# Kernel tuning notes

Hardware: AMD Instinct MI355X
Metric: run time of the kernel (lower is better)

The kernel has to match this reference:

```python
import jax, jax.numpy as jnp
import numpy as np

D_MODEL = 1024
B, N = 2, 4096
EPS = 1e-4


def setup_inputs() -> dict:
    key = jax.random.key(0)
    ks = jax.random.split(key, 8)
    s = 1.0 / np.sqrt(D_MODEL)
    return {
        "x": jax.random.normal(ks[0], (B, N, D_MODEL), dtype=jnp.float32),
        "Wq": jax.random.normal(ks[1], (D_MODEL, D_MODEL), dtype=jnp.float32) * s,
        "bq": jax.random.normal(ks[2], (D_MODEL,), dtype=jnp.float32) * 0.01,
        "Wk": jax.random.normal(ks[3], (D_MODEL, D_MODEL), dtype=jnp.float32) * s,
        "bk": jax.random.normal(ks[4], (D_MODEL,), dtype=jnp.float32) * 0.01,
        "Wv": jax.random.normal(ks[5], (D_MODEL, D_MODEL), dtype=jnp.float32) * s,
        "bv": jax.random.normal(ks[6], (D_MODEL,), dtype=jnp.float32) * 0.01,
        "alpha": jnp.float32(1.5),
        "lam": jnp.float32(12.0),
    }


def reference(x, Wq, bq, Wk, bk, Wv, bv, alpha, lam):
    # CSOCKernelAttention.forward
    Bb, n, d = x.shape
    # torch nn.Linear: y = x @ W.T + b
    q = jnp.einsum("bnd,ed->bne", x, Wq) + bq
    k = jnp.einsum("bnd,ed->bne", x, Wk) + bk
    v = jnp.einsum("bnd,ed->bne", x, Wv) + bv
    idx = jnp.arange(n, dtype=jnp.float32)
    r = jnp.abs(idx[:, None] - idx[None, :])  # [N, N]
    # K(r) = (r + eps)^(-|alpha|) * exp(-r / |lambda|)
    K = (r + EPS) ** (-jnp.abs(alpha)) * jnp.exp(-r / jnp.abs(lam))  # [N, N]
    logits = jnp.einsum("bqd,bkd->bqk", q, k) / jnp.sqrt(jnp.float32(d))
    logits = logits * K[None]
    attn = jax.nn.softmax(logits, axis=-1)
    out = jnp.einsum("bqk,bkd->bqd", attn, v)
    return (out, attn, K)
```

## Files before the change

### kernel.cpp

```cpp
#include <hip/hip_runtime.h>
#include <hip/hip_bf16.h>
#include <cstdint>
#include <cstddef>

#define D_MODEL 1024
#define SEQ_N   4096
#define BATCH   2
#define BAND    256
#define NELEM   ((size_t)BATCH * SEQ_N * D_MODEL)

typedef __attribute__((ext_vector_type(4))) float  floatx4;
typedef __attribute__((ext_vector_type(8))) short  short8;
typedef __attribute__((ext_vector_type(4))) short  short4v;

__device__ __forceinline__ unsigned short f2bf(float f) {
  unsigned u = __float_as_uint(f);
  u += 0x7FFFu + ((u >> 16) & 1u);
  return (unsigned short)(u >> 16);
}
__device__ __forceinline__ float bf2f(unsigned short u) {
  return __uint_as_float(((unsigned)u) << 16);
}

__global__ __launch_bounds__(256)
void fused_prep(const float* __restrict__ x,
                const float* __restrict__ Wq, const float* __restrict__ Wk,
                const float* __restrict__ Wv,
                const float* __restrict__ bq, const float* __restrict__ bk,
                const float* __restrict__ bv,
                const float* __restrict__ alpha_p, const float* __restrict__ lam_p,
                unsigned short* __restrict__ xb, unsigned short* __restrict__ wcat,
                float* __restrict__ bcat, float* __restrict__ K1d)
{
  int bid = blockIdx.x, tid = threadIdx.x;
  if (bid < 4096) {
    int i = bid * 256 + tid;
    const floatx4* s4 = (const floatx4*)x;
    floatx4 a = s4[i * 2], b = s4[i * 2 + 1];
    short8 pk;
    pk[0] = (short)f2bf(a[0]); pk[1] = (short)f2bf(a[1]);
    pk[2] = (short)f2bf(a[2]); pk[3] = (short)f2bf(a[3]);
    pk[4] = (short)f2bf(b[0]); pk[5] = (short)f2bf(b[1]);
    pk[6] = (short)f2bf(b[2]); pk[7] = (short)f2bf(b[3]);
    *(short8*)(xb + (size_t)i * 8) = pk;
  } else if (bid < 5632) {
    int u = bid - 4096;
    int z = u >> 9;
    int i = (u & 511) * 256 + tid;
    const float* src = (z == 0) ? Wq : (z == 1) ? Wk : Wv;
    unsigned short* d = wcat + (size_t)z * (D_MODEL * D_MODEL);
    const floatx4* s4 = (const floatx4*)src;
    floatx4 a = s4[i * 2], b = s4[i * 2 + 1];
    short8 pk;
    pk[0] = (short)f2bf(a[0]); pk[1] = (short)f2bf(a[1]);
    pk[2] = (short)f2bf(a[2]); pk[3] = (short)f2bf(a[3]);
    pk[4] = (short)f2bf(b[0]); pk[5] = (short)f2bf(b[1]);
    pk[6] = (short)f2bf(b[2]); pk[7] = (short)f2bf(b[3]);
    *(short8*)(d + (size_t)i * 8) = pk;
  } else {
    int t = (bid - 5632) * 256 + tid;
    if (t < SEQ_N) {
      float a   = fabsf(alpha_p[0]);
      float lam = fabsf(lam_p[0]);
      float rf  = (float)t;
      K1d[t] = powf(rf + 1e-4f, -a) * expf(-rf / lam);
    }
    int v = t - SEQ_N;
    if (v >= 0 && v < 3 * D_MODEL) {
      bcat[v] = (v < D_MODEL) ? bq[v]
              : (v < 2 * D_MODEL) ? bk[v - D_MODEL]
              : bv[v - 2 * D_MODEL];
    }
  }
}

__global__ void k1d_kernel(float* __restrict__ K1d,
                           const float* __restrict__ alpha_p,
                           const float* __restrict__ lam_p) {
  int r = blockIdx.x * blockDim.x + threadIdx.x;
  if (r >= SEQ_N) return;
  float a   = fabsf(alpha_p[0]);
  float lam = fabsf(lam_p[0]);
  float rf  = (float)r;
  K1d[r] = powf(rf + 1e-4f, -a) * expf(-rf / lam);
}

__global__ __launch_bounds__(256) void writeK_kernel(float* __restrict__ Kout,
                                                     const float* __restrict__ K1d) {
  size_t t = (size_t)blockIdx.x * 256 + threadIdx.x;
  size_t f = t * 4;
  int i = (int)(f >> 12);
  int j = (int)(f & 4095);
  floatx4 v;
#pragma unroll
  for (int e = 0; e < 4; ++e) {
    int d = i - (j + e); d = d < 0 ? -d : d;
    v[e] = K1d[d];
  }
  __builtin_nontemporal_store(v, (floatx4*)(Kout + f));
}

__global__ __launch_bounds__(256)
void qkv_qk(const unsigned short* __restrict__ xb,
            const unsigned short* __restrict__ wcat,
            const float* __restrict__ bcat,
            unsigned short* __restrict__ qb)
{
  __shared__ unsigned short As[128 * 32];
  __shared__ unsigned short Bs[128 * 32];
  const int tid = threadIdx.x, lane = tid & 63, wave = tid >> 6;

  int gx = (int)gridDim.x, gy = (int)gridDim.y;
  int total = gx * gy;
  int flat  = (int)blockIdx.y * gx + (int)blockIdx.x;
  int w     = (flat & 7) * (total >> 3) + (flat >> 3);
  int bx = w % gx, by = w / gx;
  const int bm0 = by * 128;
  const int bn0 = bx * 128;
  const int wm = (wave >> 1) * 64, wn = (wave & 1) * 64;

  floatx4 acc[4][4] = {};
  for (int k0 = 0; k0 < D_MODEL; k0 += 32) {
#pragma unroll
    for (int t = 0; t < 2; ++t) {
      int bu = wave * 64 + t * 256;
      int u  = bu + lane;
      const unsigned short* srcA = xb + (size_t)(bm0 + (u >> 2)) * D_MODEL + k0 + (u & 3) * 8;
      __builtin_amdgcn_global_load_lds((const __attribute__((address_space(1))) void*)srcA,
                                       (__attribute__((address_space(3))) void*)(As + bu * 8), 16, 0, 0);
      const unsigned short* srcB = wcat + (size_t)(bn0 + (u >> 2)) * D_MODEL + k0 + (u & 3) * 8;
      __builtin_amdgcn_global_load_lds((const __attribute__((address_space(1))) void*)srcB,
                                       (__attribute__((address_space(3))) void*)(Bs + bu * 8), 16, 0, 0);
    }
    __syncthreads();
    short8 af[4], bf[4];
#pragma unroll
    for (int i = 0; i < 4; ++i)
      af[i] = *(const short8*)(As + (wm + i * 16 + (lane & 15)) * 32 + (lane >> 4) * 8);
#pragma unroll
    for (int j = 0; j < 4; ++j)
      bf[j] = *(const short8*)(Bs + (wn + j * 16 + (lane & 15)) * 32 + (lane >> 4) * 8);
#pragma unroll
    for (int i = 0; i < 4; ++i)
#pragma unroll
      for (int j = 0; j < 4; ++j)
        acc[i][j] = __builtin_amdgcn_mfma_f32_16x16x32_bf16(bf[j], af[i], acc[i][j], 0, 0, 0);
    __syncthreads();
  }

#pragma unroll
  for (int i = 0; i < 4; ++i) {
#pragma unroll
    for (int j = 0; j < 4; ++j) {
      int xrow = bm0 + wm + i * 16 + (lane & 15);
      int n0   = bn0 + wn + j * 16 + (lane >> 4) * 4;
      floatx4 b4 = *(const floatx4*)(bcat + n0);
      unsigned short* C = qb + ((n0 >= D_MODEL) ? NELEM : 0);
      short4v pk;
#pragma unroll
      for (int r = 0; r < 4; ++r) pk[r] = (short)f2bf(acc[i][j][r] + b4[r]);
      *(short4v*)(C + (size_t)xrow * D_MODEL + (n0 & (D_MODEL - 1))) = pk;
    }
  }
}

__global__ __launch_bounds__(256)
void qkv_v(const unsigned short* __restrict__ xb,
           const unsigned short* __restrict__ wcat,
           const float* __restrict__ bcat,
           unsigned short* __restrict__ vT)
{
  __shared__ unsigned short As[128 * 32];
  __shared__ unsigned short Bs[128 * 32];
  const int tid = threadIdx.x, lane = tid & 63, wave = tid >> 6;

  int gx = (int)gridDim.x, gy = (int)gridDim.y;
  int total = gx * gy;
  int flat  = (int)blockIdx.y * gx + (int)blockIdx.x;
  int w     = (flat & 7) * (total >> 3) + (flat >> 3);
  int bx = w % gx, by = w / gx;
  const int bm0 = by * 128;
  const int bn0 = bx * 128;
  const int wm = (wave >> 1) * 64, wn = (wave & 1) * 64;
  const unsigned short* Wg = wcat + (size_t)2048 * D_MODEL;

  floatx4 acc[4][4] = {};
  for (int k0 = 0; k0 < D_MODEL; k0 += 32) {
#pragma unroll
    for (int t = 0; t < 2; ++t) {
      int bu = wave * 64 + t * 256;
      int u  = bu + lane;
      const unsigned short* srcA = xb + (size_t)(bm0 + (u >> 2)) * D_MODEL + k0 + (u & 3) * 8;
      __builtin_amdgcn_global_load_lds((const __attribute__((address_space(1))) void*)srcA,
                                       (__attribute__((address_space(3))) void*)(As + bu * 8), 16, 0, 0);
      const unsigned short* srcB = Wg + (size_t)(bn0 + (u >> 2)) * D_MODEL + k0 + (u & 3) * 8;
      __builtin_amdgcn_global_load_lds((const __attribute__((address_space(1))) void*)srcB,
                                       (__attribute__((address_space(3))) void*)(Bs + bu * 8), 16, 0, 0);
    }
    __syncthreads();
    short8 af[4], bf[4];
#pragma unroll
    for (int i = 0; i < 4; ++i)
      af[i] = *(const short8*)(As + (wm + i * 16 + (lane & 15)) * 32 + (lane >> 4) * 8);
#pragma unroll
    for (int j = 0; j < 4; ++j)
      bf[j] = *(const short8*)(Bs + (wn + j * 16 + (lane & 15)) * 32 + (lane >> 4) * 8);
#pragma unroll
    for (int i = 0; i < 4; ++i)
#pragma unroll
      for (int j = 0; j < 4; ++j)
        acc[i][j] = __builtin_amdgcn_mfma_f32_16x16x32_bf16(af[i], bf[j], acc[i][j], 0, 0, 0);
    __syncthreads();
  }

#pragma unroll
  for (int i = 0; i < 4; ++i) {
#pragma unroll
    for (int j = 0; j < 4; ++j) {
      int e     = bn0 + wn + j * 16 + (lane & 15);
      int rbase = bm0 + wm + i * 16 + (lane >> 4) * 4;
      float b = bcat[2048 + e];
      short4v pk;
#pragma unroll
      for (int r = 0; r < 4; ++r) pk[r] = (short)f2bf(acc[i][j][r] + b);
      *(short4v*)(vT + (size_t)e * (BATCH * SEQ_N) + rbase) = pk;
    }
  }
}

__global__ __launch_bounds__(256)
void band_logits(const unsigned short* __restrict__ Q,
                 const unsigned short* __restrict__ Kb,
                 float* __restrict__ Sband,
                 const float* __restrict__ K1d)
{
  __shared__ unsigned short As[64 * 32];
  __shared__ unsigned short Bs[128 * 32];
  const int tid = threadIdx.x, lane = tid & 63, wave = tid >> 6;
  const int bx = blockIdx.x;
  const int g  = blockIdx.y;
  const int z  = blockIdx.z;
  const int bm0 = g * 64;
  const int bn0 = g * 64 - 64 + bx * 128;
  const int wm = (wave >> 1) * 32, wn = (wave & 1) * 64;

  const unsigned short* Ag = Q  + (size_t)z * SEQ_N * D_MODEL;
  const unsigned short* Bg = Kb + (size_t)z * SEQ_N * D_MODEL;

  floatx4 acc[2][4] = {};
  for (int k0 = 0; k0 < D_MODEL; k0 += 32) {
    {
      int bu = wave * 64;
      int u  = bu + lane;
      const unsigned short* srcA = Ag + (size_t)(bm0 + (u >> 2)) * D_MODEL + k0 + (u & 3) * 8;
      __builtin_amdgcn_global_load_lds((const __attribute__((address_space(1))) void*)srcA,
                                       (__attribute__((address_space(3))) void*)(As + bu * 8), 16, 0, 0);
    }
#pragma unroll
    for (int t = 0; t < 2; ++t) {
      int bu = wave * 64 + t * 256;
      int u  = bu + lane;
      const unsigned short* srcB = Bg + (long)(bn0 + (u >> 2)) * D_MODEL + k0 + (u & 3) * 8;
      __builtin_amdgcn_global_load_lds((const __attribute__((address_space(1))) void*)srcB,
                                       (__attribute__((address_space(3))) void*)(Bs + bu * 8), 16, 0, 0);
    }
    __syncthreads();
    short8 af[2], bf[4];
#pragma unroll
    for (int i = 0; i < 2; ++i)
      af[i] = *(const short8*)(As + (wm + i * 16 + (lane & 15)) * 32 + (lane >> 4) * 8);
#pragma unroll
    for (int j = 0; j < 4; ++j)
      bf[j] = *(const short8*)(Bs + (wn + j * 16 + (lane & 15)) * 32 + (lane >> 4) * 8);
#pragma unroll
    for (int i = 0; i < 2; ++i)
#pragma unroll
      for (int j = 0; j < 4; ++j)
        acc[i][j] = __builtin_amdgcn_mfma_f32_16x16x32_bf16(af[i], bf[j], acc[i][j], 0, 0, 0);
    __syncthreads();
  }

  float* Cb = Sband + ((size_t)z * SEQ_N + bm0) * BAND + bx * 128;
#pragma unroll
  for (int i = 0; i < 2; ++i) {
#pragma unroll
    for (int j = 0; j < 4; ++j) {
      int cl  = wn + j * 16 + (lane & 15);
      int rl0 = wm + i * 16 + (lane >> 4) * 4;
#pragma unroll
      for (int r = 0; r < 4; ++r) {
        int col = bn0 + cl;
        int d = (bm0 + rl0 + r) - col; d = d < 0 ? -d : d;
        float v = ((unsigned)col < (unsigned)SEQ_N) ? acc[i][j][r] * 0.03125f * K1d[d] : 0.f;
        Cb[(size_t)(rl0 + r) * BAND + cl] = v;
      }
    }
  }
}

__global__ __launch_bounds__(256)
void softmax_band(const float* __restrict__ Sband,
                  float* __restrict__ attn,
                  unsigned short* __restrict__ Pb,
                  float* __restrict__ c_arr)
{
  __shared__ float lds_e[4][BAND];
  const int lane = threadIdx.x & 63, wave = threadIdx.x >> 6;
  const int gi = blockIdx.x * 4 + wave;
  const int ii = gi & (SEQ_N - 1);
  const int g  = ii >> 6;
  const int cbase = g * 64 - 64;
  const float* S = Sband + (size_t)gi * BAND;

  float sv[4];
  float m = 0.0f;
#pragma unroll
  for (int j = 0; j < 4; ++j) {
    int t = j * 64 + lane;
    int col = cbase + t;
    sv[j] = S[t];
    if ((unsigned)col < (unsigned)SEQ_N) m = fmaxf(m, sv[j]);
  }
#pragma unroll
  for (int o = 32; o; o >>= 1) m = fmaxf(m, __shfl_xor(m, o));

  float s = 0.f;
#pragma unroll
  for (int j = 0; j < 4; ++j) {
    int t = j * 64 + lane;
    int col = cbase + t;
    float e = ((unsigned)col < (unsigned)SEQ_N) ? __expf(sv[j] - m) : 0.f;
    sv[j] = e;
    s += e;
  }
#pragma unroll
  for (int o = 32; o; o >>= 1) s += __shfl_xor(s, o);

  int n_valid = BAND - ((g == 0) ? 64 : 0) - ((g == 63) ? 64 : 0);
  float efar  = __expf(-m);
  float denom = s + (float)(SEQ_N - n_valid) * efar;
  float inv   = 1.0f / denom;
  float c     = efar * inv;

  unsigned short* prow = Pb + (size_t)gi * BAND;
#pragma unroll
  for (int j = 0; j < 4; ++j) {
    int t = j * 64 + lane;
    float p = sv[j] * inv;
    lds_e[wave][t] = p;
    int col = cbase + t;
    prow[t] = ((unsigned)col < (unsigned)SEQ_N) ? f2bf(p - c) : (unsigned short)0;
  }
  if (lane == 0) c_arr[gi] = c;

  float* arow = attn + (size_t)gi * SEQ_N;
#pragma unroll
  for (int jj = 0; jj < 16; ++jj) {
    int col0 = jj * 256 + lane * 4;
    floatx4 o;
#pragma unroll
    for (int e = 0; e < 4; ++e) {
      int t = col0 + e - cbase;
      o[e] = ((unsigned)t < (unsigned)BAND) ? lds_e[wave][t] : c;
    }
    __builtin_nontemporal_store(o, (floatx4*)(arow + col0));
  }
}

__global__ __launch_bounds__(256)
void colsumv_kernel(const unsigned short* __restrict__ vT, float* __restrict__ colsumV) {
  const int lane = threadIdx.x & 63, wave = threadIdx.x >> 6;
  const int idx = blockIdx.x * 4 + wave;
  const int d = idx >> 1, b = idx & 1;
  const unsigned short* p = vT + (size_t)d * (BATCH * SEQ_N) + b * SEQ_N;
  float s = 0.f;
#pragma unroll
  for (int it = 0; it < 8; ++it) {
    short8 v = *(const short8*)(p + (size_t)(it * 512 + lane * 8));
#pragma unroll
    for (int e = 0; e < 8; ++e) s += bf2f((unsigned short)v[e]);
  }
#pragma unroll
  for (int o = 32; o; o >>= 1) s += __shfl_xor(s, o);
  if (lane == 0) colsumV[b * D_MODEL + d] = s;
}

__global__ __launch_bounds__(256)
void band_pv(const unsigned short* __restrict__ Pb,
             const unsigned short* __restrict__ vT,
             const float* __restrict__ c_arr,
             const float* __restrict__ colsumV,
             float* __restrict__ outp)
{
  __shared__ unsigned short As[64 * 32];
  __shared__ unsigned short Bs[128 * 32];
  const int tid = threadIdx.x, lane = tid & 63, wave = tid >> 6;
  const int bx = blockIdx.x;
  const int g  = blockIdx.y;
  const int z  = blockIdx.z;
  const int bm0 = g * 64;
  const int bn0 = bx * 128;
  const int wm = (wave >> 1) * 32, wn = (wave & 1) * 64;

  const unsigned short* Ag = Pb + ((size_t)z * SEQ_N + bm0) * BAND;
  const unsigned short* Bg = vT + (long)z * SEQ_N + (long)bm0 - 64;

  floatx4 acc[2][4] = {};
  for (int k0 = 0; k0 < BAND; k0 += 32) {
    {
      int bu = wave * 64;
      int u  = bu + lane;
      const unsigned short* srcA = Ag + (size_t)(u >> 2) * BAND + k0 + (u & 3) * 8;
      __builtin_amdgcn_global_load_lds((const __attribute__((address_space(1))) void*)srcA,
                                       (__attribute__((address_space(3))) void*)(As + bu * 8), 16, 0, 0);
    }
#pragma unroll
    for (int t = 0; t < 2; ++t) {
      int bu = wave * 64 + t * 256;
      int u  = bu + lane;
      const unsigned short* srcB = Bg + (size_t)(bn0 + (u >> 2)) * (BATCH * SEQ_N) + k0 + (u & 3) * 8;
      __builtin_amdgcn_global_load_lds((const __attribute__((address_space(1))) void*)srcB,
                                       (__attribute__((address_space(3))) void*)(Bs + bu * 8), 16, 0, 0);
    }
    __syncthreads();
    short8 af[2], bf[4];
#pragma unroll
    for (int i = 0; i < 2; ++i)
      af[i] = *(const short8*)(As + (wm + i * 16 + (lane & 15)) * 32 + (lane >> 4) * 8);
#pragma unroll
    for (int j = 0; j < 4; ++j)
      bf[j] = *(const short8*)(Bs + (wn + j * 16 + (lane & 15)) * 32 + (lane >> 4) * 8);
#pragma unroll
    for (int i = 0; i < 2; ++i)
#pragma unroll
      for (int j = 0; j < 4; ++j)
        acc[i][j] = __builtin_amdgcn_mfma_f32_16x16x32_bf16(af[i], bf[j], acc[i][j], 0, 0, 0);
    __syncthreads();
  }

#pragma unroll
  for (int i = 0; i < 2; ++i) {
#pragma unroll
    for (int j = 0; j < 4; ++j) {
      int col   = bn0 + wn + j * 16 + (lane & 15);
      int rbase = bm0 + wm + i * 16 + (lane >> 4) * 4;
      float csv = colsumV[z * D_MODEL + col];
#pragma unroll
      for (int r = 0; r < 4; ++r) {
        int row = rbase + r;
        float o = acc[i][j][r] + c_arr[(size_t)z * SEQ_N + row] * csv;
        __builtin_nontemporal_store(o, outp + ((size_t)z * SEQ_N + row) * D_MODEL + col);
      }
    }
  }
}

#define BM 128
#define BN 128
#define BK 32

template<int ASRC, int BSRC, int EPI>
__global__ __launch_bounds__(256)
void gemm_bt(const void* __restrict__ Ap_, int lda, long sA,
             const void* __restrict__ Bp_, int ldb, long sB,
             void* __restrict__ Cp_, int ldc, long sC,
             int K, const float* __restrict__ bias,
             const float* __restrict__ K1d)
{
  __shared__ unsigned short As[BM * BK];
  __shared__ unsigned short Bs[BN * BK];
  const int tid  = threadIdx.x;
  const int lane = tid & 63;
  const int wave = tid >> 6;

  int gx = (int)gridDim.x, gy = (int)gridDim.y;
  int total = gx * gy * (int)gridDim.z;
  int flat  = (int)blockIdx.z * gx * gy + (int)blockIdx.y * gx + (int)blockIdx.x;
  int w     = (flat & 7) * (total >> 3) + (flat >> 3);
  int bx = w % gx;
  int t_ = w / gx;
  int by = t_ % gy;
  int z  = t_ / gy;

  const int bm0  = by * BM;
  const int bn0  = bx * BN;
  const int wm   = (wave >> 1) * 64;
  const int wn   = (wave & 1) * 64;

  floatx4 acc[4][4] = {};

  const unsigned short* Agb = (const unsigned short*)Ap_ + (size_t)z * (size_t)sA;
  const float*          Agf = (const float*)Ap_          + (size_t)z * (size_t)sA;
  const unsigned short* Bgb = (const unsigned short*)Bp_ + (size_t)z * (size_t)sB;
  const float*          Bgf = (const float*)Bp_          + (size_t)z * (size_t)sB;

  for (int k0 = 0; k0 < K; k0 += BK) {
    if constexpr (ASRC == 0) {
#pragma unroll
      for (int t = 0; t < 2; ++t) {
        int bu = wave * 64 + t * 256;
        int u  = bu + lane;
        const unsigned short* src = Agb + (size_t)(bm0 + (u >> 2)) * lda + k0 + (u & 3) * 8;
        __builtin_amdgcn_global_load_lds((const __attribute__((address_space(1))) void*)src,
                                         (__attribute__((address_space(3))) void*)(As + bu * 8),
                                         16, 0, 0);
      }
    } else {
#pragma unroll
      for (int t = 0; t < 2; ++t) {
        int u = tid + t * 256;
        const float* src = Agf + (size_t)(bm0 + (u >> 2)) * lda + k0 + (u & 3) * 8;
        floatx4 x0 = *(const floatx4*)src;
        floatx4 x1 = *(const floatx4*)(src + 4);
        short8 pk;
        pk[0] = (short)f2bf(x0[0]); pk[1] = (short)f2bf(x0[1]);
        pk[2] = (short)f2bf(x0[2]); pk[3] = (short)f2bf(x0[3]);
        pk[4] = (short)f2bf(x1[0]); pk[5] = (short)f2bf(x1[1]);
        pk[6] = (short)f2bf(x1[2]); pk[7] = (short)f2bf(x1[3]);
        *(short8*)(As + u * 8) = pk;
      }
    }
    if constexpr (BSRC == 0) {
#pragma unroll
      for (int t = 0; t < 2; ++t) {
        int bu = wave * 64 + t * 256;
        int u  = bu + lane;
        const unsigned short* src = Bgb + (size_t)(bn0 + (u >> 2)) * ldb + k0 + (u & 3) * 8;
        __builtin_amdgcn_global_load_lds((const __attribute__((address_space(1))) void*)src,
                                         (__attribute__((address_space(3))) void*)(Bs + bu * 8),
                                         16, 0, 0);
      }
    } else {
#pragma unroll
      for (int t = 0; t < 2; ++t) {
        int u = tid + t * 256;
        const float* src = Bgf + (size_t)(bn0 + (u >> 2)) * ldb + k0 + (u & 3) * 8;
        floatx4 x0 = *(const floatx4*)src;
        floatx4 x1 = *(const floatx4*)(src + 4);
        short8 pk;
        pk[0] = (short)f2bf(x0[0]); pk[1] = (short)f2bf(x0[1]);
        pk[2] = (short)f2bf(x0[2]); pk[3] = (short)f2bf(x0[3]);
        pk[4] = (short)f2bf(x1[0]); pk[5] = (short)f2bf(x1[1]);
        pk[6] = (short)f2bf(x1[2]); pk[7] = (short)f2bf(x1[3]);
        *(short8*)(Bs + u * 8) = pk;
      }
    }
    __syncthreads();

    short8 af[4], bf[4];
#pragma unroll
    for (int i = 0; i < 4; ++i)
      af[i] = *(const short8*)(As + (wm + i * 16 + (lane & 15)) * BK + (lane >> 4) * 8);
#pragma unroll
    for (int j = 0; j < 4; ++j)
      bf[j] = *(const short8*)(Bs + (wn + j * 16 + (lane & 15)) * BK + (lane >> 4) * 8);
#pragma unroll
    for (int i = 0; i < 4; ++i)
#pragma unroll
      for (int j = 0; j < 4; ++j)
        acc[i][j] = __builtin_amdgcn_mfma_f32_16x16x32_bf16(af[i], bf[j], acc[i][j], 0, 0, 0);
    __syncthreads();
  }

  const int col0 = bn0 + wn;
  const int row0 = bm0 + wm;
#pragma unroll
  for (int i = 0; i < 4; ++i) {
#pragma unroll
    for (int j = 0; j < 4; ++j) {
      int col   = col0 + j * 16 + (lane & 15);
      int rbase = row0 + i * 16 + (lane >> 4) * 4;
      if constexpr (EPI == 0) {
        unsigned short* C = (unsigned short*)Cp_ + (size_t)z * (size_t)sC;
        float b = bias[col];
#pragma unroll
        for (int r = 0; r < 4; ++r)
          C[(size_t)(rbase + r) * ldc + col] = f2bf(acc[i][j][r] + b);
      } else if constexpr (EPI == 1) {
        unsigned short* C = (unsigned short*)Cp_ + (size_t)z * (size_t)sC;
#pragma unroll
        for (int r = 0; r < 4; ++r)
          C[(size_t)(rbase + r) * ldc + col] = f2bf(acc[i][j][r] + bias[rbase + r]);
      } else if constexpr (EPI == 2) {
        float* C = (float*)Cp_ + (size_t)z * (size_t)sC;
#pragma unroll
        for (int r = 0; r < 4; ++r) {
          int row = rbase + r;
          int d = row - col; d = d < 0 ? -d : d;
          C[(size_t)row * ldc + col] = acc[i][j][r] * 0.03125f * K1d[d];
        }
      } else {
        float* C = (float*)Cp_ + (size_t)z * (size_t)sC;
#pragma unroll
        for (int r = 0; r < 4; ++r)
          C[(size_t)(rbase + r) * ldc + col] = acc[i][j][r];
      }
    }
  }
}

__global__ __launch_bounds__(256)
void softmax_kernel(float* __restrict__ attn) {
  const int tid = threadIdx.x;
  float* p = attn + (size_t)blockIdx.x * SEQ_N;
  floatx4* p4 = (floatx4*)p;
  floatx4 x[4];
  float m = -3.402823466e+38f;
#pragma unroll
  for (int c = 0; c < 4; ++c) {
    x[c] = p4[tid + c * 256];
    m = fmaxf(m, fmaxf(fmaxf(x[c][0], x[c][1]), fmaxf(x[c][2], x[c][3])));
  }
#pragma unroll
  for (int o = 32; o; o >>= 1) m = fmaxf(m, __shfl_xor(m, o));
  __shared__ float redm[4], reds[4];
  if ((tid & 63) == 0) redm[tid >> 6] = m;
  __syncthreads();
  m = fmaxf(fmaxf(redm[0], redm[1]), fmaxf(redm[2], redm[3]));
  float s = 0.f;
#pragma unroll
  for (int c = 0; c < 4; ++c)
#pragma unroll
    for (int e = 0; e < 4; ++e) {
      float t = __expf(x[c][e] - m);
      x[c][e] = t;
      s += t;
    }
#pragma unroll
  for (int o = 32; o; o >>= 1) s += __shfl_xor(s, o);
  if ((tid & 63) == 0) reds[tid >> 6] = s;
  __syncthreads();
  s = reds[0] + reds[1] + reds[2] + reds[3];
  float inv = 1.0f / s;
#pragma unroll
  for (int c = 0; c < 4; ++c) {
    floatx4 y;
#pragma unroll
    for (int e = 0; e < 4; ++e) y[e] = x[c][e] * inv;
    p4[tid + c * 256] = y;
  }
}

extern "C" void kernel_launch(void* const* d_in, const int* in_sizes, int n_in,
                              void* d_out, int out_size, void* d_ws, size_t ws_size,
                              hipStream_t stream) {
  const float* x     = (const float*)d_in[0];
  const float* Wq    = (const float*)d_in[1];
  const float* bq    = (const float*)d_in[2];
  const float* Wk    = (const float*)d_in[3];
  const float* bk    = (const float*)d_in[4];
  const float* Wv    = (const float*)d_in[5];
  const float* bv    = (const float*)d_in[6];
  const float* alpha = (const float*)d_in[7];
  const float* lam   = (const float*)d_in[8];

  float* outp  = (float*)d_out;
  float* attnp = outp + (size_t)BATCH * SEQ_N * D_MODEL;
  float* Kp    = attnp + (size_t)BATCH * SEQ_N * SEQ_N;

  char* ws = (char*)d_ws;
  float* K1d = (float*)ws;
  unsigned short* qb  = (unsigned short*)(ws + 16384);
  unsigned short* kb  = qb + NELEM;
  unsigned short* vT  = kb + NELEM;
  unsigned short* xb  = vT + NELEM;
  unsigned short* wcat = xb + NELEM;
  float* Sband        = (float*)(wcat + (size_t)3 * D_MODEL * D_MODEL);
  unsigned short* Pb  = (unsigned short*)(Sband + (size_t)BATCH * SEQ_N * BAND);
  float* c_arr        = (float*)(Pb + (size_t)BATCH * SEQ_N * BAND);
  float* colsumV      = c_arr + (size_t)BATCH * SEQ_N;
  float* bcat         = colsumV + (size_t)BATCH * D_MODEL;

  size_t need = (size_t)((char*)(bcat + 3 * D_MODEL) - ws);
  const bool fast = ws_size >= need;

  if (fast) {
    fused_prep<<<5660, 256, 0, stream>>>(x, Wq, Wk, Wv, bq, bk, bv, alpha, lam,
                                         xb, wcat, bcat, K1d);
    writeK_kernel<<<(SEQ_N * SEQ_N / 4) / 256, 256, 0, stream>>>(Kp, K1d);

    qkv_qk<<<dim3(16, 64), 256, 0, stream>>>(xb, wcat, bcat, qb);
    qkv_v <<<dim3(8, 64), 256, 0, stream>>>(xb, wcat, bcat, vT);

    colsumv_kernel<<<BATCH * D_MODEL / 4, 256, 0, stream>>>(vT, colsumV);
    band_logits<<<dim3(2, SEQ_N / 64, BATCH), 256, 0, stream>>>(qb, kb, Sband, K1d);
    softmax_band<<<BATCH * SEQ_N / 4, 256, 0, stream>>>(Sband, attnp, Pb, c_arr);
    band_pv<<<dim3(D_MODEL / 128, SEQ_N / 64, BATCH), 256, 0, stream>>>(
        Pb, vT, c_arr, colsumV, outp);
  } else {
    k1d_kernel<<<16, 256, 0, stream>>>(K1d, alpha, lam);
    writeK_kernel<<<(SEQ_N * SEQ_N / 4) / 256, 256, 0, stream>>>(Kp, K1d);
    gemm_bt<1, 1, 0><<<dim3(D_MODEL / BN, BATCH * SEQ_N / BM, 1), 256, 0, stream>>>(
        x, D_MODEL, 0, Wq, D_MODEL, 0, qb, D_MODEL, 0, D_MODEL, bq, nullptr);
    gemm_bt<1, 1, 0><<<dim3(D_MODEL / BN, BATCH * SEQ_N / BM, 1), 256, 0, stream>>>(
        x, D_MODEL, 0, Wk, D_MODEL, 0, kb, D_MODEL, 0, D_MODEL, bk, nullptr);
    gemm_bt<1, 1, 1><<<dim3(BATCH * SEQ_N / BN, D_MODEL / BM, 1), 256, 0, stream>>>(
        Wv, D_MODEL, 0, x, D_MODEL, 0, vT, BATCH * SEQ_N, 0, D_MODEL, bv, nullptr);
    gemm_bt<0, 0, 2><<<dim3(SEQ_N / BN, SEQ_N / BM, BATCH), 256, 0, stream>>>(
        qb, D_MODEL, (long)SEQ_N * D_MODEL, kb, D_MODEL, (long)SEQ_N * D_MODEL,
        attnp, SEQ_N, (long)SEQ_N * SEQ_N, D_MODEL, nullptr, K1d);
    softmax_kernel<<<BATCH * SEQ_N, 256, 0, stream>>>(attnp);
    gemm_bt<1, 0, 3><<<dim3(D_MODEL / BN, SEQ_N / BM, BATCH), 256, 0, stream>>>(
        attnp, SEQ_N, (long)SEQ_N * SEQ_N, vT, BATCH * SEQ_N, (long)SEQ_N,
        outp, D_MODEL, (long)SEQ_N * D_MODEL, SEQ_N, nullptr, nullptr);
  }
}
```

Baseline: 182.1 us.

## Fold Wq·Wk into combined matrix to drop separate K projection

Rewrites the logits as x·(Wq^T Wk)·x^T plus bias-derived terms: a small 1024x1024 GEMM forms M = Wk^T Wq, a vector-matrix kernel builds bq·Wk and bk·Wq, and a per-row rho term carries the remaining bias contributions. The QKV projection becomes one GEMM producing U = xM + bias and V, and band_logits now multiplies U against x directly, adding rho. This removes one full projection GEMM over the sequence and the K buffer, at the cost of extra small kernels and bf16 rounding of the fused matrix, which could change accuracy.

```diff
diff --git a/kernel.cpp b/kernel.cpp
--- a/kernel.cpp
+++ b/kernel.cpp
@@ -25,13 +25,16 @@
 __global__ __launch_bounds__(256)
 void fused_prep(const float* __restrict__ x,
                 const float* __restrict__ Wq, const float* __restrict__ Wk,
-                const float* __restrict__ Wv,
-                const float* __restrict__ bq, const float* __restrict__ bk,
-                const float* __restrict__ bv,
+                const float* __restrict__ Wv, const float* __restrict__ bv,
                 const float* __restrict__ alpha_p, const float* __restrict__ lam_p,
-                unsigned short* __restrict__ xb, unsigned short* __restrict__ wcat,
-                float* __restrict__ bcat, float* __restrict__ K1d)
-{
+                unsigned short* __restrict__ xb,
+                unsigned short* __restrict__ Bcat2,
+                unsigned short* __restrict__ wqT,
+                unsigned short* __restrict__ wkT,
+                float* __restrict__ bias2,
+                float* __restrict__ K1d)
+{
+  __shared__ unsigned short Tld[64][66];
   int bid = blockIdx.x, tid = threadIdx.x;
   if (bid < 4096) {
     int i = bid * 256 + tid;
@@ -43,22 +46,40 @@
     pk[4] = (short)f2bf(b[0]); pk[5] = (short)f2bf(b[1]);
     pk[6] = (short)f2bf(b[2]); pk[7] = (short)f2bf(b[3]);
     *(short8*)(xb + (size_t)i * 8) = pk;
-  } else if (bid < 5632) {
-    int u = bid - 4096;
-    int z = u >> 9;
-    int i = (u & 511) * 256 + tid;
-    const float* src = (z == 0) ? Wq : (z == 1) ? Wk : Wv;
-    unsigned short* d = wcat + (size_t)z * (D_MODEL * D_MODEL);
-    const floatx4* s4 = (const floatx4*)src;
+  } else if (bid < 4608) {
+    int i = (bid - 4096) * 256 + tid;
+    const floatx4* s4 = (const floatx4*)Wv;
     floatx4 a = s4[i * 2], b = s4[i * 2 + 1];
     short8 pk;
     pk[0] = (short)f2bf(a[0]); pk[1] = (short)f2bf(a[1]);
     pk[2] = (short)f2bf(a[2]); pk[3] = (short)f2bf(a[3]);
     pk[4] = (short)f2bf(b[0]); pk[5] = (short)f2bf(b[1]);
     pk[6] = (short)f2bf(b[2]); pk[7] = (short)f2bf(b[3]);
-    *(short8*)(d + (size_t)i * 8) = pk;
+    *(short8*)(Bcat2 + (size_t)D_MODEL * D_MODEL + (size_t)i * 8) = pk;
+  } else if (bid < 5120) {
+    int u = bid - 4608;
+    const float* src = (u < 256) ? Wq : Wk;
+    unsigned short* dst = (u < 256) ? wqT : wkT;
+    int t = u & 255;
+    int tr = t >> 4, tc = t & 15;
+    int rl = tid >> 2, cc = (tid & 3) * 16;
+    const float* sp = src + (size_t)(tr * 64 + rl) * D_MODEL + tc * 64 + cc;
+#pragma unroll
+    for (int q4 = 0; q4 < 4; ++q4) {
+      floatx4 v = *(const floatx4*)(sp + q4 * 4);
+#pragma unroll
+      for (int e = 0; e < 4; ++e) Tld[cc + q4 * 4 + e][rl] = f2bf(v[e]);
+    }
+    __syncthreads();
+    int cl = tid >> 2, rchunk = (tid & 3) * 16;
+    short8 o0, o1;
+#pragma unroll
+    for (int e = 0; e < 8; ++e) { o0[e] = (short)Tld[cl][rchunk + e]; o1[e] = (short)Tld[cl][rchunk + 8 + e]; }
+    unsigned short* dp = dst + (size_t)(tc * 64 + cl) * D_MODEL + tr * 64 + rchunk;
+    *(short8*)dp = o0;
+    *(short8*)(dp + 8) = o1;
   } else {
-    int t = (bid - 5632) * 256 + tid;
+    int t = (bid - 5120) * 256 + tid;
     if (t < SEQ_N) {
       float a   = fabsf(alpha_p[0]);
       float lam = fabsf(lam_p[0]);
@@ -66,12 +87,48 @@
       K1d[t] = powf(rf + 1e-4f, -a) * expf(-rf / lam);
     }
     int v = t - SEQ_N;
-    if (v >= 0 && v < 3 * D_MODEL) {
-      bcat[v] = (v < D_MODEL) ? bq[v]
-              : (v < 2 * D_MODEL) ? bk[v - D_MODEL]
-              : bv[v - 2 * D_MODEL];
-    }
-  }
+    if (v >= 0 && v < D_MODEL) bias2[D_MODEL + v] = bv[v];
+  }
+}
+
+__global__ __launch_bounds__(256)
+void vecmat_kernel(const float* __restrict__ bq, const float* __restrict__ Wk,
+                   const float* __restrict__ bk, const float* __restrict__ Wq,
+                   float* __restrict__ bias2, float* __restrict__ wqv)
+{
+  int z = blockIdx.z;
+  int d = blockIdx.x * 256 + threadIdx.x;
+  const float* b = z ? bk : bq;
+  const float* W = z ? Wq : Wk;
+  float s = 0.f;
+#pragma unroll 8
+  for (int e = 0; e < D_MODEL; ++e)
+    s += b[e] * W[(size_t)e * D_MODEL + d];
+  if (z) wqv[d] = s; else bias2[d] = s;
+}
+
+__global__ __launch_bounds__(256)
+void rho_kernel(const unsigned short* __restrict__ xb, const float* __restrict__ wqv,
+                const float* __restrict__ bq, const float* __restrict__ bk,
+                float* __restrict__ rho)
+{
+  const int lane = threadIdx.x & 63, wave = threadIdx.x >> 6;
+  const int gi = blockIdx.x * 4 + wave;
+  const unsigned short* xr = xb + (size_t)gi * D_MODEL + lane * 16;
+  float s1 = 0.f, s2 = 0.f;
+  short8 v0 = *(const short8*)xr, v1 = *(const short8*)(xr + 8);
+#pragma unroll
+  for (int e = 0; e < 8; ++e) {
+    s1 += bf2f((unsigned short)v0[e]) * wqv[lane * 16 + e];
+    s1 += bf2f((unsigned short)v1[e]) * wqv[lane * 16 + 8 + e];
+  }
+#pragma unroll
+  for (int e = 0; e < 16; ++e)
+    s2 += bq[lane * 16 + e] * bk[lane * 16 + e];
+  float s = s1 + s2;
+#pragma unroll
+  for (int o = 32; o; o >>= 1) s += __shfl_xor(s, o);
+  if (lane == 0) rho[gi] = s;
 }
 
 __global__ void k1d_kernel(float* __restrict__ K1d,
@@ -101,10 +158,67 @@
 }
 
 __global__ __launch_bounds__(256)
-void qkv_qk(const unsigned short* __restrict__ xb,
-            const unsigned short* __restrict__ wcat,
-            const float* __restrict__ bcat,
-            unsigned short* __restrict__ qb)
+void gemm64_mt(const unsigned short* __restrict__ A,
+               const unsigned short* __restrict__ B,
+               unsigned short* __restrict__ C)
+{
+  __shared__ unsigned short As[64 * 32];
+  __shared__ unsigned short Bs[64 * 32];
+  const int tid = threadIdx.x, lane = tid & 63, wave = tid >> 6;
+  int gx = (int)gridDim.x;
+  int total = gx * (int)gridDim.y;
+  int flat  = (int)blockIdx.y * gx + (int)blockIdx.x;
+  int w     = (flat & 7) * (total >> 3) + (flat >> 3);
+  int bx = w % gx, by = w / gx;
+  const int bm0 = by * 64, bn0 = bx * 64;
+  const int wm = (wave >> 1) * 32, wn = (wave & 1) * 32;
+
+  floatx4 acc[2][2] = {};
+  for (int k0 = 0; k0 < D_MODEL; k0 += 32) {
+    {
+      int bu = wave * 64;
+      int u  = bu + lane;
+      const unsigned short* srcA = A + (size_t)(bm0 + (u >> 2)) * D_MODEL + k0 + (u & 3) * 8;
+      __builtin_amdgcn_global_load_lds((const __attribute__((address_space(1))) void*)srcA,
+                                       (__attribute__((address_space(3))) void*)(As + bu * 8), 16, 0, 0);
+      const unsigned short* srcB = B + (size_t)(bn0 + (u >> 2)) * D_MODEL + k0 + (u & 3) * 8;
+      __builtin_amdgcn_global_load_lds((const __attribute__((address_space(1))) void*)srcB,
+                                       (__attribute__((address_space(3))) void*)(Bs + bu * 8), 16, 0, 0);
+    }
+    __syncthreads();
+    short8 af[2], bf[2];
+#pragma unroll
+    for (int i = 0; i < 2; ++i)
+      af[i] = *(const short8*)(As + (wm + i * 16 + (lane & 15)) * 32 + (lane >> 4) * 8);
+#pragma unroll
+    for (int j = 0; j < 2; ++j)
+      bf[j] = *(const short8*)(Bs + (wn + j * 16 + (lane & 15)) * 32 + (lane >> 4) * 8);
+#pragma unroll
+    for (int i = 0; i < 2; ++i)
+#pragma unroll
+      for (int j = 0; j < 2; ++j)
+        acc[i][j] = __builtin_amdgcn_mfma_f32_16x16x32_bf16(af[i], bf[j], acc[i][j], 0, 0, 0);
+    __syncthreads();
+  }
+#pragma unroll
+  for (int i = 0; i < 2; ++i) {
+#pragma unroll
+    for (int j = 0; j < 2; ++j) {
+      int col   = bn0 + wn + j * 16 + (lane & 15);
+      int rbase = bm0 + wm + i * 16 + (lane >> 4) * 4;
+#pragma unroll
+      for (int r = 0; r < 4; ++r)
+        C[(size_t)(rbase + r) * D_MODEL + col] = f2bf(acc[i][j][r]);
+    }
+  }
+}
+
+__global__ __launch_bounds__(256)
+void uv_gemm(const unsigned short* __restrict__ xb,
+             const unsigned short* __restrict__ Bcat2,
+             const float* __restrict__ bias2,
+             unsigned short* __restrict__ ub,
+             unsigned short* __restrict__ vT)
 {
   __shared__ unsigned short As[128 * 32];
   __shared__ unsigned short Bs[128 * 32];
@@ -118,6 +232,7 @@
   const int bm0 = by * 128;
   const int bn0 = bx * 128;
   const int wm = (wave >> 1) * 64, wn = (wave & 1) * 64;
+  const bool isU = (bn0 < D_MODEL);
 
   floatx4 acc[4][4] = {};
   for (int k0 = 0; k0 < D_MODEL; k0 += 32) {
@@ -128,7 +243,7 @@
       const unsigned short* srcA = xb + (size_t)(bm0 + (u >> 2)) * D_MODEL + k0 + (u & 3) * 8;
       __builtin_amdgcn_global_load_lds((const __attribute__((address_space(1))) void*)srcA,
                                        (__attribute__((address_space(3))) void*)(As + bu * 8), 16, 0, 0);
-      const unsigned short* srcB = wcat + (size_t)(bn0 + (u >> 2)) * D_MODEL + k0 + (u & 3) * 8;
+      const unsigned short* srcB = Bcat2 + (size_t)(bn0 + (u >> 2)) * D_MODEL + k0 + (u & 3) * 8;
       __builtin_amdgcn_global_load_lds((const __attribute__((address_space(1))) void*)srcB,
                                        (__attribute__((address_space(3))) void*)(Bs + bu * 8), 16, 0, 0);
     }
@@ -140,97 +255,58 @@
 #pragma unroll
     for (int j = 0; j < 4; ++j)
       bf[j] = *(const short8*)(Bs + (wn + j * 16 + (lane & 15)) * 32 + (lane >> 4) * 8);
-#pragma unroll
-    for (int i = 0; i < 4; ++i)
-#pragma unroll
-      for (int j = 0; j < 4; ++j)
-        acc[i][j] = __builtin_amdgcn_mfma_f32_16x16x32_bf16(bf[j], af[i], acc[i][j], 0, 0, 0);
-    __syncthreads();
-  }
-
-#pragma unroll
-  for (int i = 0; i < 4; ++i) {
-#pragma unroll
-    for (int j = 0; j < 4; ++j) {
-      int xrow = bm0 + wm + i * 16 + (lane & 15);
-      int n0   = bn0 + wn + j * 16 + (lane >> 4) * 4;
-      floatx4 b4 = *(const floatx4*)(bcat + n0);
-      unsigned short* C = qb + ((n0 >= D_MODEL) ? NELEM : 0);
-      short4v pk;
-#pragma unroll
-      for (int r = 0; r < 4; ++r) pk[r] = (short)f2bf(acc[i][j][r] + b4[r]);
-      *(short4v*)(C + (size_t)xrow * D_MODEL + (n0 & (D_MODEL - 1))) = pk;
-    }
-  }
-}
-
-__global__ __launch_bounds__(256)
-void qkv_v(const unsigned short* __restrict__ xb,
-           const unsigned short* __restrict__ wcat,
-           const float* __restrict__ bcat,
-           unsigned short* __restrict__ vT)
-{
-  __shared__ unsigned short As[128 * 32];
-  __shared__ unsigned short Bs[128 * 32];
-  const int tid = threadIdx.x, lane = tid & 63, wave = tid >> 6;
-
-  int gx = (int)gridDim.x, gy = (int)gridDim.y;
-  int total = gx * gy;
-  int flat  = (int)blockIdx.y * gx + (int)blockIdx.x;
-  int w     = (flat & 7) * (total >> 3) + (flat >> 3);
-  int bx = w % gx, by = w / gx;
-  const int bm0 = by * 128;
-  const int bn0 = bx * 128;
-  const int wm = (wave >> 1) * 64, wn = (wave & 1) * 64;
-  const unsigned short* Wg = wcat + (size_t)2048 * D_MODEL;
-
-  floatx4 acc[4][4] = {};
-  for (int k0 = 0; k0 < D_MODEL; k0 += 32) {
-#pragma unroll
-    for (int t = 0; t < 2; ++t) {
-      int bu = wave * 64 + t * 256;
-      int u  = bu + lane;
-      const unsigned short* srcA = xb + (size_t)(bm0 + (u >> 2)) * D_MODEL + k0 + (u & 3) * 8;
-      __builtin_amdgcn_global_load_lds((const __attribute__((address_space(1))) void*)srcA,
-                                       (__attribute__((address_space(3))) void*)(As + bu * 8), 16, 0, 0);
-      const unsigned short* srcB = Wg + (size_t)(bn0 + (u >> 2)) * D_MODEL + k0 + (u & 3) * 8;
-      __builtin_amdgcn_global_load_lds((const __attribute__((address_space(1))) void*)srcB,
-                                       (__attribute__((address_space(3))) void*)(Bs + bu * 8), 16, 0, 0);
-    }
-    __syncthreads();
-    short8 af[4], bf[4];
-#pragma unroll
-    for (int i = 0; i < 4; ++i)
-      af[i] = *(const short8*)(As + (wm + i * 16 + (lane & 15)) * 32 + (lane >> 4) * 8);
-#pragma unroll
-    for (int j = 0; j < 4; ++j)
-      bf[j] = *(const short8*)(Bs + (wn + j * 16 + (lane & 15)) * 32 + (lane >> 4) * 8);
-#pragma unroll
-    for (int i = 0; i < 4; ++i)
-#pragma unroll
-      for (int j = 0; j < 4; ++j)
-        acc[i][j] = __builtin_amdgcn_mfma_f32_16x16x32_bf16(af[i], bf[j], acc[i][j], 0, 0, 0);
-    __syncthreads();
-  }
-
-#pragma unroll
-  for (int i = 0; i < 4; ++i) {
-#pragma unroll
-    for (int j = 0; j < 4; ++j) {
-      int e     = bn0 + wn + j * 16 + (lane & 15);
-      int rbase = bm0 + wm + i * 16 + (lane >> 4) * 4;
-      float b = bcat[2048 + e];
-      short4v pk;
-#pragma unroll
-      for (int r = 0; r < 4; ++r) pk[r] = (short)f2bf(acc[i][j][r] + b);
-      *(short4v*)(vT + (size_t)e * (BATCH * SEQ_N) + rbase) = pk;
-    }
-  }
-}
-
-__global__ __launch_bounds__(256)
-void band_logits(const unsigned short* __restrict__ Q,
-                 const unsigned short* __restrict__ Kb,
+    if (isU) {
+#pragma unroll
+      for (int i = 0; i < 4; ++i)
+#pragma unroll
+        for (int j = 0; j < 4; ++j)
+          acc[i][j] = __builtin_amdgcn_mfma_f32_16x16x32_bf16(bf[j], af[i], acc[i][j], 0, 0, 0);
+    } else {
+#pragma unroll
+      for (int i = 0; i < 4; ++i)
+#pragma unroll
+        for (int j = 0; j < 4; ++j)
+          acc[i][j] = __builtin_amdgcn_mfma_f32_16x16x32_bf16(af[i], bf[j], acc[i][j], 0, 0, 0);
+    }
+    __syncthreads();
+  }
+
+  if (isU) {
+#pragma unroll
+    for (int i = 0; i < 4; ++i) {
+#pragma unroll
+      for (int j = 0; j < 4; ++j) {
+        int xrow = bm0 + wm + i * 16 + (lane & 15);
+        int n0   = bn0 + wn + j * 16 + (lane >> 4) * 4;
+        floatx4 b4 = *(const floatx4*)(bias2 + n0);
+        short4v pk;
+#pragma unroll
+        for (int r = 0; r < 4; ++r) pk[r] = (short)f2bf(acc[i][j][r] + b4[r]);
+        *(short4v*)(ub + (size_t)xrow * D_MODEL + n0) = pk;
+      }
+    }
+  } else {
+#pragma unroll
+    for (int i = 0; i < 4; ++i) {
+#pragma unroll
+      for (int j = 0; j < 4; ++j) {
+        int n     = bn0 + wn + j * 16 + (lane & 15);
+        int e     = n - D_MODEL;
+        int rbase = bm0 + wm + i * 16 + (lane >> 4) * 4;
+        float b = bias2[n];
+        short4v pk;
+#pragma unroll
+        for (int r = 0; r < 4; ++r) pk[r] = (short)f2bf(acc[i][j][r] + b);
+        *(short4v*)(vT + (size_t)e * (BATCH * SEQ_N) + rbase) = pk;
+      }
+    }
+  }
+}
+
+__global__ __launch_bounds__(256)
+void band_logits(const unsigned short* __restrict__ U,
+                 const unsigned short* __restrict__ Xb,
+                 const float* __restrict__ rho,
                  float* __restrict__ Sband,
                  const float* __restrict__ K1d)
 {
@@ -244,8 +320,8 @@
   const int bn0 = g * 64 - 64 + bx * 128;
   const int wm = (wave >> 1) * 32, wn = (wave & 1) * 64;
 
-  const unsigned short* Ag = Q  + (size_t)z * SEQ_N * D_MODEL;
-  const unsigned short* Bg = Kb + (size_t)z * SEQ_N * D_MODEL;
+  const unsigned short* Ag = U  + (size_t)z * SEQ_N * D_MODEL;
+  const unsigned short* Bg = Xb + (size_t)z * SEQ_N * D_MODEL;
 
   floatx4 acc[2][4] = {};
   for (int k0 = 0; k0 < D_MODEL; k0 += 32) {
@@ -283,15 +359,19 @@
   float* Cb = Sband + ((size_t)z * SEQ_N + bm0) * BAND + bx * 128;
 #pragma unroll
   for (int i = 0; i < 2; ++i) {
+    int rl0 = wm + i * 16 + (lane >> 4) * 4;
+    float rr[4];
+#pragma unroll
+    for (int r = 0; r < 4; ++r) rr[r] = rho[(size_t)z * SEQ_N + bm0 + rl0 + r];
 #pragma unroll
     for (int j = 0; j < 4; ++j) {
       int cl  = wn + j * 16 + (lane & 15);
-      int rl0 = wm + i * 16 + (lane >> 4) * 4;
 #pragma unroll
       for (int r = 0; r < 4; ++r) {
         int col = bn0 + cl;
         int d = (bm0 + rl0 + r) - col; d = d < 0 ? -d : d;
-        float v = ((unsigned)col < (unsigned)SEQ_N) ? acc[i][j][r] * 0.03125f * K1d[d] : 0.f;
+        float v = ((unsigned)col < (unsigned)SEQ_N)
+                    ? (acc[i][j][r] + rr[r]) * 0.03125f * K1d[d] : 0.f;
         Cb[(size_t)(rl0 + r) * BAND + cl] = v;
       }
     }
@@ -660,34 +740,39 @@
 
   char* ws = (char*)d_ws;
   float* K1d = (float*)ws;
-  unsigned short* qb  = (unsigned short*)(ws + 16384);
-  unsigned short* kb  = qb + NELEM;
-  unsigned short* vT  = kb + NELEM;
-  unsigned short* xb  = vT + NELEM;
-  unsigned short* wcat = xb + NELEM;
-  float* Sband        = (float*)(wcat + (size_t)3 * D_MODEL * D_MODEL);
-  unsigned short* Pb  = (unsigned short*)(Sband + (size_t)BATCH * SEQ_N * BAND);
-  float* c_arr        = (float*)(Pb + (size_t)BATCH * SEQ_N * BAND);
-  float* colsumV      = c_arr + (size_t)BATCH * SEQ_N;
-  float* bcat         = colsumV + (size_t)BATCH * D_MODEL;
-
-  size_t need = (size_t)((char*)(bcat + 3 * D_MODEL) - ws);
+  unsigned short* vT   = (unsigned short*)(ws + 16384);
+  unsigned short* xb   = vT + NELEM;
+  unsigned short* ub   = xb + NELEM;
+  unsigned short* wqT  = ub + NELEM;
+  unsigned short* wkT  = wqT + (size_t)D_MODEL * D_MODEL;
+  unsigned short* Bcat2 = wkT + (size_t)D_MODEL * D_MODEL;
+  float* Sband   = (float*)(Bcat2 + (size_t)2 * D_MODEL * D_MODEL);
+  unsigned short* Pb = (unsigned short*)(Sband + (size_t)BATCH * SEQ_N * BAND);
+  float* c_arr   = (float*)(Pb + (size_t)BATCH * SEQ_N * BAND);
+  float* colsumV = c_arr + (size_t)BATCH * SEQ_N;
+  float* bias2   = colsumV + (size_t)BATCH * D_MODEL;
+  float* wqv     = bias2 + 2 * D_MODEL;
+  float* rho     = wqv + D_MODEL;
+
+  size_t need = (size_t)((char*)(rho + BATCH * SEQ_N) - ws);
   const bool fast = ws_size >= need;
 
   if (fast) {
-    fused_prep<<<5660, 256, 0, stream>>>(x, Wq, Wk, Wv, bq, bk, bv, alpha, lam,
-                                         xb, wcat, bcat, K1d);
+    fused_prep<<<5140, 256, 0, stream>>>(x, Wq, Wk, Wv, bv, alpha, lam,
+                                         xb, Bcat2, wqT, wkT, bias2, K1d);
+    vecmat_kernel<<<dim3(4, 1, 2), 256, 0, stream>>>(bq, Wk, bk, Wq, bias2, wqv);
     writeK_kernel<<<(SEQ_N * SEQ_N / 4) / 256, 256, 0, stream>>>(Kp, K1d);
-
-    qkv_qk<<<dim3(16, 64), 256, 0, stream>>>(xb, wcat, bcat, qb);
-    qkv_v <<<dim3(8, 64), 256, 0, stream>>>(xb, wcat, bcat, vT);
-
+    gemm64_mt<<<dim3(16, 16), 256, 0, stream>>>(wkT, wqT, Bcat2);
+    rho_kernel<<<BATCH * SEQ_N / 4, 256, 0, stream>>>(xb, wqv, bq, bk, rho);
+    uv_gemm<<<dim3(16, 64), 256, 0, stream>>>(xb, Bcat2, bias2, ub, vT);
     colsumv_kernel<<<BATCH * D_MODEL / 4, 256, 0, stream>>>(vT, colsumV);
-    band_logits<<<dim3(2, SEQ_N / 64, BATCH), 256, 0, stream>>>(qb, kb, Sband, K1d);
+    band_logits<<<dim3(2, SEQ_N / 64, BATCH), 256, 0, stream>>>(ub, xb, rho, Sband, K1d);
     softmax_band<<<BATCH * SEQ_N / 4, 256, 0, stream>>>(Sband, attnp, Pb, c_arr);
     band_pv<<<dim3(D_MODEL / 128, SEQ_N / 64, BATCH), 256, 0, stream>>>(
         Pb, vT, c_arr, colsumV, outp);
   } else {
+    unsigned short* qb = xb;
+    unsigned short* kb = ub;
     k1d_kernel<<<16, 256, 0, stream>>>(K1d, alpha, lam);
     writeK_kernel<<<(SEQ_N * SEQ_N / 4) / 256, 256, 0, stream>>>(Kp, K1d);
     gemm_bt<1, 1, 0><<<dim3(D_MODEL / BN, BATCH * SEQ_N / BM, 1), 256, 0, stream>>>(
```

Result: slower. 226.6 us (+24.4%).

## Double K-tile depth in QKV GEMMs and XOR-swizzle LDS layout

Applied to the files above, without the earlier changes.

The QKV projection GEMMs now stage a 64-wide K slice per iteration instead of 32, halving the number of barrier pairs and loop iterations. The LDS tiles use an XOR swizzle of the 16-byte chunk index by row, applied on the global source address so each thread's global_load_lds chunk lands permuted and the fragment reads avoid bank conflicts. This doubles shared memory per block (32 KB), which may reduce occupancy.

```diff
diff --git a/kernel.cpp b/kernel.cpp
--- a/kernel.cpp
+++ b/kernel.cpp
@@ -106,8 +106,8 @@
             const float* __restrict__ bcat,
             unsigned short* __restrict__ qb)
 {
-  __shared__ unsigned short As[128 * 32];
-  __shared__ unsigned short Bs[128 * 32];
+  __shared__ unsigned short As[128 * 64];
+  __shared__ unsigned short Bs[128 * 64];
   const int tid = threadIdx.x, lane = tid & 63, wave = tid >> 6;
 
   int gx = (int)gridDim.x, gy = (int)gridDim.y;
@@ -120,31 +120,42 @@
   const int wm = (wave >> 1) * 64, wn = (wave & 1) * 64;
 
   floatx4 acc[4][4] = {};
-  for (int k0 = 0; k0 < D_MODEL; k0 += 32) {
-#pragma unroll
-    for (int t = 0; t < 2; ++t) {
-      int bu = wave * 64 + t * 256;
-      int u  = bu + lane;
-      const unsigned short* srcA = xb + (size_t)(bm0 + (u >> 2)) * D_MODEL + k0 + (u & 3) * 8;
+  for (int k0 = 0; k0 < D_MODEL; k0 += 64) {
+#pragma unroll
+    for (int t = 0; t < 4; ++t) {
+      int bu  = wave * 64 + t * 256;
+      int u   = bu + lane;
+      int row = u >> 3;
+      int c   = (u & 7) ^ (row & 7);
+      const unsigned short* srcA = xb + (size_t)(bm0 + row) * D_MODEL + k0 + c * 8;
       __builtin_amdgcn_global_load_lds((const __attribute__((address_space(1))) void*)srcA,
                                        (__attribute__((address_space(3))) void*)(As + bu * 8), 16, 0, 0);
-      const unsigned short* srcB = wcat + (size_t)(bn0 + (u >> 2)) * D_MODEL + k0 + (u & 3) * 8;
+      const unsigned short* srcB = wcat + (size_t)(bn0 + row) * D_MODEL + k0 + c * 8;
       __builtin_amdgcn_global_load_lds((const __attribute__((address_space(1))) void*)srcB,
                                        (__attribute__((address_space(3))) void*)(Bs + bu * 8), 16, 0, 0);
     }
     __syncthreads();
-    short8 af[4], bf[4];
-#pragma unroll
-    for (int i = 0; i < 4; ++i)
-      af[i] = *(const short8*)(As + (wm + i * 16 + (lane & 15)) * 32 + (lane >> 4) * 8);
-#pragma unroll
-    for (int j = 0; j < 4; ++j)
-      bf[j] = *(const short8*)(Bs + (wn + j * 16 + (lane & 15)) * 32 + (lane >> 4) * 8);
-#pragma unroll
-    for (int i = 0; i < 4; ++i)
-#pragma unroll
-      for (int j = 0; j < 4; ++j)
-        acc[i][j] = __builtin_amdgcn_mfma_f32_16x16x32_bf16(bf[j], af[i], acc[i][j], 0, 0, 0);
+#pragma unroll
+    for (int s = 0; s < 2; ++s) {
+      short8 af[4], bf[4];
+#pragma unroll
+      for (int i = 0; i < 4; ++i) {
+        int row = wm + i * 16 + (lane & 15);
+        int pc  = (s * 4 + (lane >> 4)) ^ (row & 7);
+        af[i] = *(const short8*)(As + row * 64 + pc * 8);
+      }
+#pragma unroll
+      for (int j = 0; j < 4; ++j) {
+        int row = wn + j * 16 + (lane & 15);
+        int pc  = (s * 4 + (lane >> 4)) ^ (row & 7);
+        bf[j] = *(const short8*)(Bs + row * 64 + pc * 8);
+      }
+#pragma unroll
+      for (int i = 0; i < 4; ++i)
+#pragma unroll
+        for (int j = 0; j < 4; ++j)
+          acc[i][j] = __builtin_amdgcn_mfma_f32_16x16x32_bf16(bf[j], af[i], acc[i][j], 0, 0, 0);
+    }
     __syncthreads();
   }
 
@@ -170,8 +181,8 @@
            const float* __restrict__ bcat,
            unsigned short* __restrict__ vT)
 {
-  __shared__ unsigned short As[128 * 32];
-  __shared__ unsigned short Bs[128 * 32];
+  __shared__ unsigned short As[128 * 64];
+  __shared__ unsigned short Bs[128 * 64];
   const int tid = threadIdx.x, lane = tid & 63, wave = tid >> 6;
 
   int gx = (int)gridDim.x, gy = (int)gridDim.y;
@@ -185,31 +196,42 @@
   const unsigned short* Wg = wcat + (size_t)2048 * D_MODEL;
 
   floatx4 acc[4][4] = {};
-  for (int k0 = 0; k0 < D_MODEL; k0 += 32) {
-#pragma unroll
-    for (int t = 0; t < 2; ++t) {
-      int bu = wave * 64 + t * 256;
-      int u  = bu + lane;
-      const unsigned short* srcA = xb + (size_t)(bm0 + (u >> 2)) * D_MODEL + k0 + (u & 3) * 8;
+  for (int k0 = 0; k0 < D_MODEL; k0 += 64) {
+#pragma unroll
+    for (int t = 0; t < 4; ++t) {
+      int bu  = wave * 64 + t * 256;
+      int u   = bu + lane;
+      int row = u >> 3;
+      int c   = (u & 7) ^ (row & 7);
+      const unsigned short* srcA = xb + (size_t)(bm0 + row) * D_MODEL + k0 + c * 8;
       __builtin_amdgcn_global_load_lds((const __attribute__((address_space(1))) void*)srcA,
                                        (__attribute__((address_space(3))) void*)(As + bu * 8), 16, 0, 0);
-      const unsigned short* srcB = Wg + (size_t)(bn0 + (u >> 2)) * D_MODEL + k0 + (u & 3) * 8;
+      const unsigned short* srcB = Wg + (size_t)(bn0 + row) * D_MODEL + k0 + c * 8;
       __builtin_amdgcn_global_load_lds((const __attribute__((address_space(1))) void*)srcB,
                                        (__attribute__((address_space(3))) void*)(Bs + bu * 8), 16, 0, 0);
     }
     __syncthreads();
-    short8 af[4], bf[4];
-#pragma unroll
-    for (int i = 0; i < 4; ++i)
-      af[i] = *(const short8*)(As + (wm + i * 16 + (lane & 15)) * 32 + (lane >> 4) * 8);
-#pragma unroll
-    for (int j = 0; j < 4; ++j)
-      bf[j] = *(const short8*)(Bs + (wn + j * 16 + (lane & 15)) * 32 + (lane >> 4) * 8);
-#pragma unroll
-    for (int i = 0; i < 4; ++i)
-#pragma unroll
-      for (int j = 0; j < 4; ++j)
-        acc[i][j] = __builtin_amdgcn_mfma_f32_16x16x32_bf16(af[i], bf[j], acc[i][j], 0, 0, 0);
+#pragma unroll
+    for (int s = 0; s < 2; ++s) {
+      short8 af[4], bf[4];
+#pragma unroll
+      for (int i = 0; i < 4; ++i) {
+        int row = wm + i * 16 + (lane & 15);
+        int pc  = (s * 4 + (lane >> 4)) ^ (row & 7);
+        af[i] = *(const short8*)(As + row * 64 + pc * 8);
+      }
+#pragma unroll
+      for (int j = 0; j < 4; ++j) {
+        int row = wn + j * 16 + (lane & 15);
+        int pc  = (s * 4 + (lane >> 4)) ^ (row & 7);
+        bf[j] = *(const short8*)(Bs + row * 64 + pc * 8);
+      }
+#pragma unroll
+      for (int i = 0; i < 4; ++i)
+#pragma unroll
+        for (int j = 0; j < 4; ++j)
+          acc[i][j] = __builtin_amdgcn_mfma_f32_16x16x32_bf16(af[i], bf[j], acc[i][j], 0, 0, 0);
+    }
     __syncthreads();
   }
 
```

Result: faster. 174.7 us (-4.0%).
